# Optimization experiments

Hardware: AMD Instinct MI355X
Metric: run time of the kernel (lower is better)

The kernel has to match this reference:

```python
import jax, jax.numpy as jnp
import numpy as np

NEIGHBORS = 16  # init kwarg 'neighbors'


def _mlp(x, params):
    # SetTransform with reduction='none': pointwise MLP, ReLU between layers, linear output
    for W, b in params[:-1]:
        x = jax.nn.relu(x @ W + b)
    W, b = params[-1]
    return x @ W + b


def setup_inputs() -> dict:
    key = jax.random.key(0)
    B, K, P, DIM, C_IN = 4, 2048, 4096, 3, 64
    C_MID, C_OUT = 32, 128
    WH = 32          # weight_hidden sizes
    FH = 256         # final_hidden size
    FIN = C_IN * C_MID  # 2048, final_conv input

    ks = jax.random.split(key, 16)

    def lin(k, fan_in, fan_out):
        k1, k2 = jax.random.split(k)
        s = 1.0 / np.sqrt(fan_in)
        W = jax.random.uniform(k1, (fan_in, fan_out), minval=-s, maxval=s, dtype=jnp.float32)
        b = jax.random.uniform(k2, (fan_out,), minval=-s, maxval=s, dtype=jnp.float32)
        return W, b

    wc0_W, wc0_b = lin(ks[0], DIM, WH)
    wc1_W, wc1_b = lin(ks[1], WH, WH)
    wc2_W, wc2_b = lin(ks[2], WH, C_MID)
    fc0_W, fc0_b = lin(ks[3], FIN, FH)
    fc1_W, fc1_b = lin(ks[4], FH, C_OUT)

    return {
        "keys": jax.random.normal(ks[5], (B, K, DIM), dtype=jnp.float32),
        "points": jax.random.normal(ks[6], (B, P, DIM), dtype=jnp.float32),
        "feats": jax.random.normal(ks[7], (B, P, C_IN), dtype=jnp.float32),
        "wc0_W": wc0_W, "wc0_b": wc0_b,
        "wc1_W": wc1_W, "wc1_b": wc1_b,
        "wc2_W": wc2_W, "wc2_b": wc2_b,
        "fc0_W": fc0_W, "fc0_b": fc0_b,
        "fc1_W": fc1_W, "fc1_b": fc1_b,
    }


def reference(keys, points, feats,
              wc0_W, wc0_b, wc1_W, wc1_b, wc2_W, wc2_b,
              fc0_W, fc0_b, fc1_W, fc1_b):
    B, K, _ = keys.shape
    # Euclidean dist_fn: rel_pos [B,K,P,dim], squared dist [B,K,P]; all points valid
    dist_vec = points[:, None, :, :] - keys[:, :, None, :]
    dist = jnp.sum(dist_vec * dist_vec, axis=-1)
    # k smallest distances -> neighbor indices [B,K,N]
    _, idxs = jax.lax.top_k(-dist, NEIGHBORS)
    # gather relative positions [B,K,N,dim] and neighbor features [B,K,N,c_in]
    neighbor_rel = jnp.take_along_axis(dist_vec, idxs[..., None], axis=2)
    b_idx = jnp.arange(B)[:, None, None]
    neighbor_feats = feats[b_idx, idxs]
    # per-edge weight MLP: [B,K,N,dim] -> [B,K,N,c_mid]
    m = _mlp(neighbor_rel, [(wc0_W, wc0_b), (wc1_W, wc1_b), (wc2_W, wc2_b)])
    # masked matmul aggregation (all neighbors valid under euclidean dist_fn):
    # m^T @ neighbor_feats -> [B,K,c_mid,c_in], flattened to [B,K,c_mid*c_in]
    e = jnp.einsum('bknm,bknc->bkmc', m, neighbor_feats).reshape(B, K, -1)
    # final pointwise MLP -> [B,K,c_out]
    return _mlp(e, [(fc0_W, fc0_b), (fc1_W, fc1_b)])
```

## Files before the change

### kernel.cpp

```cpp
#include <hip/hip_runtime.h>
#include <cfloat>
#include <climits>

#define BATCH 4
#define KQ    2048
#define NP    4096
#define CIN   64
#define CMID  32
#define NB    16
#define NBINS 4096
#define CANDCAP 256
#define QPB   4

typedef short   bf16x8  __attribute__((ext_vector_type(8)));
typedef float   floatx4 __attribute__((ext_vector_type(4)));

__device__ __forceinline__ unsigned short f2bf(float f) {
  unsigned u = __float_as_uint(f);
  u = (u + 0x7fffu + ((u >> 16) & 1u)) >> 16;
  return (unsigned short)u;
}
__device__ __forceinline__ float bf2f(unsigned short u) {
  return __uint_as_float((unsigned)u << 16);
}

__device__ __forceinline__ void load_lds16(const void* g, void* l) {
  __builtin_amdgcn_global_load_lds(
      (const __attribute__((address_space(1))) unsigned int*)g,
      (__attribute__((address_space(3))) unsigned int*)l, 16, 0, 0);
}

__global__ __launch_bounds__(256, 8) void select_topk(
    const float* __restrict__ keys, const float* __restrict__ points,
    int* __restrict__ nidx_g) {
  __shared__ __align__(16) int hist[NBINS];
  __shared__ int   psum[256];
  __shared__ float cand_d[CANDCAP];
  __shared__ int   cand_i[CANDCAP];
  __shared__ int   nidx[NB];
  __shared__ int   sel_cnt, cand_cnt, sBin, sCbelow;

  const int tid = threadIdx.x;
  const int b   = blockIdx.x >> 11;

#pragma unroll
  for (int t = 0; t < 4; ++t)
    *reinterpret_cast<int4*>(&hist[(tid + t * 256) * 4]) = int4{0, 0, 0, 0};
  if (tid == 0) { sel_cnt = 0; cand_cnt = 0; }

  const float kx = keys[blockIdx.x * 3 + 0];
  const float ky = keys[blockIdx.x * 3 + 1];
  const float kz = keys[blockIdx.x * 3 + 2];
  __syncthreads();

  const float4* pv =
      reinterpret_cast<const float4*>(points + (size_t)b * NP * 3) + (size_t)tid * 12;
  float dreg[16];
#pragma unroll
  for (int g = 0; g < 4; ++g) {
    const float4 v0 = pv[g * 3 + 0];
    const float4 v1 = pv[g * 3 + 1];
    const float4 v2 = pv[g * 3 + 2];
    const float px[4] = {v0.x, v0.w, v1.z, v2.y};
    const float py[4] = {v0.y, v1.x, v1.w, v2.z};
    const float pz[4] = {v0.z, v1.y, v2.x, v2.w};
#pragma unroll
    for (int j = 0; j < 4; ++j) {
      const float dx = px[j] - kx, dy = py[j] - ky, dz = pz[j] - kz;
      const float d  = dx * dx + dy * dy + dz * dz;
      dreg[g * 4 + j] = d;
      atomicAdd(&hist[__float_as_uint(d) >> 19], 1);
    }
  }
  __syncthreads();

  {
    const int base = tid * 16;
    int s = 0;
#pragma unroll
    for (int t = 0; t < 4; ++t) {
      const int4 hv = *reinterpret_cast<const int4*>(&hist[base + t * 4]);
      s += hv.x + hv.y + hv.z + hv.w;
    }
    psum[tid] = s;
  }
  __syncthreads();

  if (tid < 64) {
    const int q = psum[tid * 4] + psum[tid * 4 + 1] + psum[tid * 4 + 2] + psum[tid * 4 + 3];
    int incl = q;
#pragma unroll
    for (int off = 1; off < 64; off <<= 1) {
      int u = __shfl_up(incl, off);
      if (tid >= off) incl += u;
    }
    unsigned long long bal = __ballot(incl >= NB);
    int firstlane = __ffsll((long long)bal) - 1;
    if (tid == firstlane) {
      int cum = incl - q;
      int bin = -1;
      for (int t = 0; t < 4 && bin < 0; ++t) {
        const int ps = psum[tid * 4 + t];
        if (cum + ps >= NB) {
          const int b0 = (tid * 4 + t) * 16;
          for (int j = 0; j < 16; ++j) {
            const int h = hist[b0 + j];
            if (cum + h >= NB) { bin = b0 + j; break; }
            cum += h;
          }
        } else cum += ps;
      }
      sBin = bin; sCbelow = cum;
    }
  }
  __syncthreads();

  const unsigned B = (unsigned)sBin;
#pragma unroll
  for (int j = 0; j < 16; ++j) {
    const int i = tid * 16 + j;
    const unsigned bk = __float_as_uint(dreg[j]) >> 19;
    if (bk < B) {
      int pos = atomicAdd(&sel_cnt, 1);
      nidx[pos] = i;
    } else if (bk == B) {
      int pos = atomicAdd(&cand_cnt, 1);
      if (pos < CANDCAP) { cand_d[pos] = dreg[j]; cand_i[pos] = i; }
    }
  }
  __syncthreads();

  {
    const int rem = NB - sCbelow;
    const int cc  = min(cand_cnt, CANDCAP);
    for (int j = tid; j < cc; j += 256) {
      const float dj = cand_d[j]; const int ij = cand_i[j];
      int rank = 0;
      for (int k = 0; k < cc; ++k) {
        const float dk = cand_d[k]; const int ik = cand_i[k];
        rank += (dk < dj || (dk == dj && ik < ij)) ? 1 : 0;
      }
      if (rank < rem) nidx[sCbelow + rank] = ij;
    }
  }
  __syncthreads();

  if (tid < NB) nidx_g[blockIdx.x * NB + tid] = nidx[tid];
}

__global__ __launch_bounds__(256) void edge_prep(
    const float* __restrict__ keys, const float* __restrict__ points,
    const float* __restrict__ feats, const int* __restrict__ nidx_g,
    const float* __restrict__ wc0_W, const float* __restrict__ wc0_b,
    const float* __restrict__ wc1_W, const float* __restrict__ wc1_b,
    const float* __restrict__ wc2_W, const float* __restrict__ wc2_b,
    const float* __restrict__ fc0_W, const float* __restrict__ fc1_W,
    unsigned short* __restrict__ W0T, unsigned short* __restrict__ W1T,
    unsigned short* __restrict__ E) {
  __shared__ __align__(16) float w0[96], b0v[32], w1[1024], b1v[32], w2[1024], b2v[32];
  __shared__ int   idx_s[QPB * NB];
  __shared__ __align__(16) unsigned short m_bf[QPB * NB][40];
  __shared__ __align__(16) char u_mem[64 * 144];
  float (*h2_all)[36]        = reinterpret_cast<float(*)[36]>(u_mem);
  unsigned short (*f_bf)[72] = reinterpret_cast<unsigned short(*)[72]>(u_mem);
  float (*tt)[33]            = reinterpret_cast<float(*)[33]>(u_mem);

  const int tid = threadIdx.x;
  const int bid = blockIdx.x;
  const int q0  = bid * QPB;
  const int b   = q0 >> 11;

  if (bid < 544) {
    const float* W; unsigned short* WT; int K, N, k0, n0;
    if (bid < 512) { W = fc0_W; WT = W0T; K = 2048; N = 256;
                     k0 = (bid >> 3) * 32; n0 = (bid & 7) * 32; }
    else           { W = fc1_W; WT = W1T; K = 256;  N = 128;
                     k0 = ((bid - 512) >> 2) * 32; n0 = ((bid - 512) & 3) * 32; }
    const int tx = tid & 31, ty = tid >> 5;
#pragma unroll
    for (int p = 0; p < 4; ++p)
      tt[ty + p * 8][tx] = W[(size_t)(k0 + ty + p * 8) * N + n0 + tx];
    __syncthreads();
#pragma unroll
    for (int p = 0; p < 4; ++p)
      WT[(size_t)(n0 + ty + p * 8) * K + k0 + tx] = f2bf(tt[tx][ty + p * 8]);
    __syncthreads();
  }

  if (tid < 96) w0[tid] = wc0_W[tid];
  for (int i = tid; i < 1024; i += 256) { w1[i] = wc1_W[i]; w2[i] = wc2_W[i]; }
  if (tid < 32) { b0v[tid] = wc0_b[tid]; b1v[tid] = wc1_b[tid]; b2v[tid] = wc2_b[tid]; }
  if (tid < QPB * NB) idx_s[tid] = nidx_g[q0 * NB + tid];
  __syncthreads();

  const int edge = tid & 63;
  const int qt   = tid >> 6;
  const int ob   = qt * 8;
  const int qe   = edge >> 4;
  const int idx  = idx_s[edge];
  {
    const float* p  = points + ((size_t)b * NP + idx) * 3;
    const float* kq = keys + (size_t)(q0 + qe) * 3;
    const float rx = p[0] - kq[0], ry = p[1] - kq[1], rz = p[2] - kq[2];

    float h1[32];
#pragma unroll
    for (int o4 = 0; o4 < 8; ++o4) {
      const float4 a = *reinterpret_cast<const float4*>(&w0[o4 * 4]);
      const float4 c = *reinterpret_cast<const float4*>(&w0[32 + o4 * 4]);
      const float4 d = *reinterpret_cast<const float4*>(&w0[64 + o4 * 4]);
      const float4 e = *reinterpret_cast<const float4*>(&b0v[o4 * 4]);
      h1[o4 * 4 + 0] = fmaxf(0.f, rx * a.x + ry * c.x + rz * d.x + e.x);
      h1[o4 * 4 + 1] = fmaxf(0.f, rx * a.y + ry * c.y + rz * d.y + e.y);
      h1[o4 * 4 + 2] = fmaxf(0.f, rx * a.z + ry * c.z + rz * d.z + e.z);
      h1[o4 * 4 + 3] = fmaxf(0.f, rx * a.w + ry * c.w + rz * d.w + e.w);
    }

    float acc2[8];
#pragma unroll
    for (int j = 0; j < 8; ++j) acc2[j] = b1v[ob + j];
#pragma unroll
    for (int i = 0; i < 32; ++i) {
      const float hv = h1[i];
#pragma unroll
      for (int j4 = 0; j4 < 2; ++j4) {
        const float4 w = *reinterpret_cast<const float4*>(&w1[i * 32 + ob + j4 * 4]);
        acc2[j4 * 4 + 0] += hv * w.x;
        acc2[j4 * 4 + 1] += hv * w.y;
        acc2[j4 * 4 + 2] += hv * w.z;
        acc2[j4 * 4 + 3] += hv * w.w;
      }
    }
#pragma unroll
    for (int j4 = 0; j4 < 2; ++j4) {
      float4 o4v;
      o4v.x = fmaxf(acc2[j4 * 4 + 0], 0.f);
      o4v.y = fmaxf(acc2[j4 * 4 + 1], 0.f);
      o4v.z = fmaxf(acc2[j4 * 4 + 2], 0.f);
      o4v.w = fmaxf(acc2[j4 * 4 + 3], 0.f);
      *reinterpret_cast<float4*>(&h2_all[edge][ob + j4 * 4]) = o4v;
    }
  }
  __syncthreads();

  float mo[8];
#pragma unroll
  for (int j = 0; j < 8; ++j) mo[j] = b2v[ob + j];
#pragma unroll
  for (int i = 0; i < 32; ++i) {
    const float hv = h2_all[edge][i];
#pragma unroll
    for (int j4 = 0; j4 < 2; ++j4) {
      const float4 w = *reinterpret_cast<const float4*>(&w2[i * 32 + ob + j4 * 4]);
      mo[j4 * 4 + 0] += hv * w.x;
      mo[j4 * 4 + 1] += hv * w.y;
      mo[j4 * 4 + 2] += hv * w.z;
      mo[j4 * 4 + 3] += hv * w.w;
    }
  }
#pragma unroll
  for (int j = 0; j < 4; ++j) {
    const unsigned lo = f2bf(mo[2 * j]), hi = f2bf(mo[2 * j + 1]);
    *reinterpret_cast<unsigned*>(&m_bf[edge][ob + 2 * j]) = lo | (hi << 16);
  }
  __syncthreads();

#pragma unroll
  for (int t = 0; t < 4; ++t) {
    const int task = tid + t * 256;
    const int row = task >> 4, ch = task & 15;
    const float4 v = *reinterpret_cast<const float4*>(
        feats + ((size_t)b * NP + idx_s[row]) * CIN + ch * 4);
    ushort4 o4;
    o4.x = f2bf(v.x); o4.y = f2bf(v.y); o4.z = f2bf(v.z); o4.w = f2bf(v.w);
    *reinterpret_cast<ushort4*>(&f_bf[row][ch * 4]) = o4;
  }
  __syncthreads();

  const int wv = tid >> 6, lane = tid & 63;
  const int co = lane & 7, mg = lane >> 3;
  {
    const int q = wv;
    float acc[4][8] = {};
#pragma unroll
    for (int n = 0; n < 16; ++n) {
      const int row = q * 16 + n;
      const ushort4 m4 = *reinterpret_cast<const ushort4*>(&m_bf[row][mg * 4]);
      const float mv[4] = {bf2f(m4.x), bf2f(m4.y), bf2f(m4.z), bf2f(m4.w)};
      const uint4 fv = *reinterpret_cast<const uint4*>(&f_bf[row][co * 8]);
      float fc[8];
      fc[0] = __uint_as_float(fv.x << 16); fc[1] = __uint_as_float(fv.x & 0xffff0000u);
      fc[2] = __uint_as_float(fv.y << 16); fc[3] = __uint_as_float(fv.y & 0xffff0000u);
      fc[4] = __uint_as_float(fv.z << 16); fc[5] = __uint_as_float(fv.z & 0xffff0000u);
      fc[6] = __uint_as_float(fv.w << 16); fc[7] = __uint_as_float(fv.w & 0xffff0000u);
#pragma unroll
      for (int i = 0; i < 4; ++i)
#pragma unroll
        for (int j = 0; j < 8; ++j) acc[i][j] += mv[i] * fc[j];
    }
    unsigned short* Eq = E + (size_t)(q0 + q) * 2048;
#pragma unroll
    for (int i = 0; i < 4; ++i) {
      const int mid = mg * 4 + i;
      uint4 o;
      o.x = (unsigned)f2bf(acc[i][0]) | ((unsigned)f2bf(acc[i][1]) << 16);
      o.y = (unsigned)f2bf(acc[i][2]) | ((unsigned)f2bf(acc[i][3]) << 16);
      o.z = (unsigned)f2bf(acc[i][4]) | ((unsigned)f2bf(acc[i][5]) << 16);
      o.w = (unsigned)f2bf(acc[i][6]) | ((unsigned)f2bf(acc[i][7]) << 16);
      *reinterpret_cast<uint4*>(&Eq[mid * 64 + co * 8]) = o;
    }
  }
}

template <int KDIM, bool RELU, bool OUTBF16, bool SWIZZLE>
__global__ __launch_bounds__(256) void gemm_mfma(
    const unsigned short* __restrict__ A,
    const unsigned short* __restrict__ Bt,
    const float* __restrict__ bias,
    void* __restrict__ Cout, int ldc) {
  __shared__ __align__(16) unsigned short Al[2][64 * 128];
  __shared__ __align__(16) unsigned short Bl[2][64 * 128];
  const int tid  = threadIdx.x;
  int m0, n0;
  if (SWIZZLE) {
    const int L    = blockIdx.x;
    const int slot = L >> 3;
    m0 = ((L & 7) * 16 + (slot >> 2)) * 64;
    n0 = (slot & 3) * 64;
  } else {
    m0 = blockIdx.x * 64;
    n0 = blockIdx.y * 64;
  }
  const int wv   = tid >> 6, lane = tid & 63;
  const int quad = lane >> 4, s = lane & 15;
  const int moff = (wv & 1) * 32, noff = (wv >> 1) * 32;
  const int lr   = lane >> 4, lc = lane & 15;

  floatx4 acc[2][2] = {{{0.f,0.f,0.f,0.f},{0.f,0.f,0.f,0.f}},
                       {{0.f,0.f,0.f,0.f},{0.f,0.f,0.f,0.f}}};

  auto stage = [&](int buf, int k0) {
#pragma unroll
    for (int t = 0; t < 4; ++t) {
      const int R0 = wv * 16 + t * 4;
      const int r  = R0 + lr;
      const int gc = lc ^ (r & 7);
      load_lds16(A  + (size_t)(m0 + r) * KDIM + k0 + gc * 8, &Al[buf][R0 * 128]);
      load_lds16(Bt + (size_t)(n0 + r) * KDIM + k0 + gc * 8, &Bl[buf][R0 * 128]);
    }
  };

  auto compute = [&](int buf) {
#pragma unroll
    for (int h = 0; h < 4; ++h) {
      bf16x8 af[2], bfr[2];
#pragma unroll
      for (int i = 0; i < 2; ++i) {
        const int r = moff + i * 16 + s;
        af[i] = *reinterpret_cast<const bf16x8*>(
            &Al[buf][(size_t)r * 128 + ((((h << 2) | quad) ^ (r & 7)) << 3)]);
      }
#pragma unroll
      for (int j = 0; j < 2; ++j) {
        const int r = noff + j * 16 + s;
        bfr[j] = *reinterpret_cast<const bf16x8*>(
            &Bl[buf][(size_t)r * 128 + ((((h << 2) | quad) ^ (r & 7)) << 3)]);
      }
#pragma unroll
      for (int i = 0; i < 2; ++i)
#pragma unroll
        for (int j = 0; j < 2; ++j)
          acc[i][j] = __builtin_amdgcn_mfma_f32_16x16x32_bf16(af[i], bfr[j], acc[i][j], 0, 0, 0);
    }
  };

  constexpr int NT = KDIM / 128;

  stage(0, 0);
  __syncthreads();
  int cur = 0;
#pragma unroll 1
  for (int it = 0; it < NT - 1; ++it) {
    stage(cur ^ 1, (it + 1) * 128);
    compute(cur);
    __syncthreads();
    cur ^= 1;
  }
  compute(cur);

#pragma unroll
  for (int i = 0; i < 2; ++i)
#pragma unroll
    for (int j = 0; j < 2; ++j) {
      const int col = n0 + noff + j * 16 + s;
      const float bv = bias[col];
#pragma unroll
      for (int r = 0; r < 4; ++r) {
        const int row = m0 + moff + i * 16 + quad * 4 + r;
        float v = acc[i][j][r] + bv;
        if (RELU) v = fmaxf(v, 0.f);
        if (OUTBF16)
          ((unsigned short*)Cout)[(size_t)row * ldc + col] = f2bf(v);
        else
          ((float*)Cout)[(size_t)row * ldc + col] = v;
      }
    }
}

extern "C" void kernel_launch(void* const* d_in, const int* in_sizes, int n_in,
                              void* d_out, int out_size, void* d_ws, size_t ws_size,
                              hipStream_t stream) {
  const float* keys   = (const float*)d_in[0];
  const float* points = (const float*)d_in[1];
  const float* feats  = (const float*)d_in[2];
  const float* wc0_W  = (const float*)d_in[3];
  const float* wc0_b  = (const float*)d_in[4];
  const float* wc1_W  = (const float*)d_in[5];
  const float* wc1_b  = (const float*)d_in[6];
  const float* wc2_W  = (const float*)d_in[7];
  const float* wc2_b  = (const float*)d_in[8];
  const float* fc0_W  = (const float*)d_in[9];
  const float* fc0_b  = (const float*)d_in[10];
  const float* fc1_W  = (const float*)d_in[11];
  const float* fc1_b  = (const float*)d_in[12];
  float* out = (float*)d_out;

  const int M = BATCH * KQ;
  char* ws = (char*)d_ws;
  unsigned short* E    = (unsigned short*)(ws);
  unsigned short* H16  = (unsigned short*)(ws + (size_t)33554432);
  unsigned short* W0T  = (unsigned short*)(ws + (size_t)37748736);
  unsigned short* W1T  = (unsigned short*)(ws + (size_t)38797312);
  int*            nidx = (int*)(ws + (size_t)38862848);

  select_topk<<<M, 256, 0, stream>>>(keys, points, nidx);
  edge_prep<<<M / QPB, 256, 0, stream>>>(keys, points, feats, nidx,
                                         wc0_W, wc0_b, wc1_W, wc1_b, wc2_W, wc2_b,
                                         fc0_W, fc1_W, W0T, W1T, E);
  gemm_mfma<2048, true,  true,  true ><<<512, 256, 0, stream>>>(E, W0T, fc0_b, H16, 256);
  gemm_mfma<256,  false, false, false><<<dim3(M / 64, 2), 256, 0, stream>>>(H16, W1T, fc1_b, out, 128);
}
```

Baseline: 170.7 us.

## Rewrite edge MLP and aggregation in edge_prep with per-wave bf16 MFMA

```diff
diff --git a/kernel.cpp b/kernel.cpp
--- a/kernel.cpp
+++ b/kernel.cpp
@@ -157,18 +157,12 @@
     const float* __restrict__ fc0_W, const float* __restrict__ fc1_W,
     unsigned short* __restrict__ W0T, unsigned short* __restrict__ W1T,
     unsigned short* __restrict__ E) {
-  __shared__ __align__(16) float w0[96], b0v[32], w1[1024], b1v[32], w2[1024], b2v[32];
-  __shared__ int   idx_s[QPB * NB];
-  __shared__ __align__(16) unsigned short m_bf[QPB * NB][40];
-  __shared__ __align__(16) char u_mem[64 * 144];
-  float (*h2_all)[36]        = reinterpret_cast<float(*)[36]>(u_mem);
-  unsigned short (*f_bf)[72] = reinterpret_cast<unsigned short(*)[72]>(u_mem);
-  float (*tt)[33]            = reinterpret_cast<float(*)[33]>(u_mem);
+  __shared__ __align__(16) char smem[4 * 5888];
+  float (*tt)[33] = reinterpret_cast<float(*)[33]>(smem);
 
   const int tid = threadIdx.x;
   const int bid = blockIdx.x;
   const int q0  = bid * QPB;
-  const int b   = q0 >> 11;
 
   if (bid < 544) {
     const float* W; unsigned short* WT; int K, N, k0, n0;
@@ -187,127 +181,99 @@
     __syncthreads();
   }
 
-  if (tid < 96) w0[tid] = wc0_W[tid];
-  for (int i = tid; i < 1024; i += 256) { w1[i] = wc1_W[i]; w2[i] = wc2_W[i]; }
-  if (tid < 32) { b0v[tid] = wc0_b[tid]; b1v[tid] = wc1_b[tid]; b2v[tid] = wc2_b[tid]; }
-  if (tid < QPB * NB) idx_s[tid] = nidx_g[q0 * NB + tid];
-  __syncthreads();
-
-  const int edge = tid & 63;
-  const int qt   = tid >> 6;
-  const int ob   = qt * 8;
-  const int qe   = edge >> 4;
-  const int idx  = idx_s[edge];
-  {
-    const float* p  = points + ((size_t)b * NP + idx) * 3;
-    const float* kq = keys + (size_t)(q0 + qe) * 3;
-    const float rx = p[0] - kq[0], ry = p[1] - kq[1], rz = p[2] - kq[2];
-
-    float h1[32];
-#pragma unroll
-    for (int o4 = 0; o4 < 8; ++o4) {
-      const float4 a = *reinterpret_cast<const float4*>(&w0[o4 * 4]);
-      const float4 c = *reinterpret_cast<const float4*>(&w0[32 + o4 * 4]);
-      const float4 d = *reinterpret_cast<const float4*>(&w0[64 + o4 * 4]);
-      const float4 e = *reinterpret_cast<const float4*>(&b0v[o4 * 4]);
-      h1[o4 * 4 + 0] = fmaxf(0.f, rx * a.x + ry * c.x + rz * d.x + e.x);
-      h1[o4 * 4 + 1] = fmaxf(0.f, rx * a.y + ry * c.y + rz * d.y + e.y);
-      h1[o4 * 4 + 2] = fmaxf(0.f, rx * a.z + ry * c.z + rz * d.z + e.z);
-      h1[o4 * 4 + 3] = fmaxf(0.f, rx * a.w + ry * c.w + rz * d.w + e.w);
-    }
-
-    float acc2[8];
-#pragma unroll
-    for (int j = 0; j < 8; ++j) acc2[j] = b1v[ob + j];
-#pragma unroll
-    for (int i = 0; i < 32; ++i) {
-      const float hv = h1[i];
-#pragma unroll
-      for (int j4 = 0; j4 < 2; ++j4) {
-        const float4 w = *reinterpret_cast<const float4*>(&w1[i * 32 + ob + j4 * 4]);
-        acc2[j4 * 4 + 0] += hv * w.x;
-        acc2[j4 * 4 + 1] += hv * w.y;
-        acc2[j4 * 4 + 2] += hv * w.z;
-        acc2[j4 * 4 + 3] += hv * w.w;
-      }
-    }
-#pragma unroll
-    for (int j4 = 0; j4 < 2; ++j4) {
-      float4 o4v;
-      o4v.x = fmaxf(acc2[j4 * 4 + 0], 0.f);
-      o4v.y = fmaxf(acc2[j4 * 4 + 1], 0.f);
-      o4v.z = fmaxf(acc2[j4 * 4 + 2], 0.f);
-      o4v.w = fmaxf(acc2[j4 * 4 + 3], 0.f);
-      *reinterpret_cast<float4*>(&h2_all[edge][ob + j4 * 4]) = o4v;
-    }
-  }
-  __syncthreads();
-
-  float mo[8];
-#pragma unroll
-  for (int j = 0; j < 8; ++j) mo[j] = b2v[ob + j];
-#pragma unroll
-  for (int i = 0; i < 32; ++i) {
-    const float hv = h2_all[edge][i];
-#pragma unroll
-    for (int j4 = 0; j4 < 2; ++j4) {
-      const float4 w = *reinterpret_cast<const float4*>(&w2[i * 32 + ob + j4 * 4]);
-      mo[j4 * 4 + 0] += hv * w.x;
-      mo[j4 * 4 + 1] += hv * w.y;
-      mo[j4 * 4 + 2] += hv * w.z;
-      mo[j4 * 4 + 3] += hv * w.w;
-    }
-  }
-#pragma unroll
-  for (int j = 0; j < 4; ++j) {
-    const unsigned lo = f2bf(mo[2 * j]), hi = f2bf(mo[2 * j + 1]);
-    *reinterpret_cast<unsigned*>(&m_bf[edge][ob + 2 * j]) = lo | (hi << 16);
-  }
-  __syncthreads();
+  const int wv   = tid >> 6, lane = tid & 63;
+  const int s    = lane & 15, g = lane >> 4;
+  const int q    = q0 + wv;
+  const int b    = q >> 11;
+
+  unsigned short* h2s = reinterpret_cast<unsigned short*>(smem + wv * 5888);
+  unsigned short* ms  = reinterpret_cast<unsigned short*>(smem + wv * 5888 + 1280);
+  unsigned short* fsT = reinterpret_cast<unsigned short*>(smem + wv * 5888 + 2816);
+
+  bf16x8 B1[2], B2[2];
+#pragma unroll
+  for (int t = 0; t < 2; ++t) {
+#pragma unroll
+    for (int e = 0; e < 8; ++e) {
+      const int k = 8 * g + e, c = s + 16 * t;
+      B1[t][e] = (short)f2bf(wc1_W[k * 32 + c]);
+      B2[t][e] = (short)f2bf(wc2_W[k * 32 + c]);
+    }
+  }
+
+  const int idx = nidx_g[q * NB + s];
+  const float* p = points + ((size_t)b * NP + idx) * 3;
+  const float kx = keys[q * 3], ky = keys[q * 3 + 1], kz = keys[q * 3 + 2];
+  const float rx = p[0] - kx, ry = p[1] - ky, rz = p[2] - kz;
+  bf16x8 A1;
+#pragma unroll
+  for (int e = 0; e < 8; ++e) {
+    const int j = 8 * g + e;
+    float h = rx * wc0_W[j] + ry * wc0_W[32 + j] + rz * wc0_W[64 + j] + wc0_b[j];
+    A1[e] = (short)f2bf(fmaxf(h, 0.f));
+  }
+
+  const floatx4 zc = {0.f, 0.f, 0.f, 0.f};
+
+#pragma unroll
+  for (int t = 0; t < 2; ++t) {
+    floatx4 d = __builtin_amdgcn_mfma_f32_16x16x32_bf16(A1, B1[t], zc, 0, 0, 0);
+    const float bv = wc1_b[s + 16 * t];
+#pragma unroll
+    for (int r = 0; r < 4; ++r)
+      h2s[(g * 4 + r) * 40 + 16 * t + s] = f2bf(fmaxf(d[r] + bv, 0.f));
+  }
+
+  const bf16x8 A2 = *reinterpret_cast<const bf16x8*>(&h2s[s * 40 + g * 8]);
+
+#pragma unroll
+  for (int t = 0; t < 2; ++t) {
+    floatx4 d = __builtin_amdgcn_mfma_f32_16x16x32_bf16(A2, B2[t], zc, 0, 0, 0);
+    const float bv = wc2_b[s + 16 * t];
+    ushort4 o;
+    o.x = f2bf(d[0] + bv); o.y = f2bf(d[1] + bv);
+    o.z = f2bf(d[2] + bv); o.w = f2bf(d[3] + bv);
+    *reinterpret_cast<ushort4*>(&ms[(16 * t + s) * 24 + g * 4]) = o;
+  }
 
 #pragma unroll
   for (int t = 0; t < 4; ++t) {
-    const int task = tid + t * 256;
-    const int row = task >> 4, ch = task & 15;
+    const int chunk = g + 4 * t;
+    const int n = s;
+    const int idx_n = nidx_g[q * NB + n];
     const float4 v = *reinterpret_cast<const float4*>(
-        feats + ((size_t)b * NP + idx_s[row]) * CIN + ch * 4);
-    ushort4 o4;
-    o4.x = f2bf(v.x); o4.y = f2bf(v.y); o4.z = f2bf(v.z); o4.w = f2bf(v.w);
-    *reinterpret_cast<ushort4*>(&f_bf[row][ch * 4]) = o4;
-  }
-  __syncthreads();
-
-  const int wv = tid >> 6, lane = tid & 63;
-  const int co = lane & 7, mg = lane >> 3;
-  {
-    const int q = wv;
-    float acc[4][8] = {};
-#pragma unroll
-    for (int n = 0; n < 16; ++n) {
-      const int row = q * 16 + n;
-      const ushort4 m4 = *reinterpret_cast<const ushort4*>(&m_bf[row][mg * 4]);
-      const float mv[4] = {bf2f(m4.x), bf2f(m4.y), bf2f(m4.z), bf2f(m4.w)};
-      const uint4 fv = *reinterpret_cast<const uint4*>(&f_bf[row][co * 8]);
-      float fc[8];
-      fc[0] = __uint_as_float(fv.x << 16); fc[1] = __uint_as_float(fv.x & 0xffff0000u);
-      fc[2] = __uint_as_float(fv.y << 16); fc[3] = __uint_as_float(fv.y & 0xffff0000u);
-      fc[4] = __uint_as_float(fv.z << 16); fc[5] = __uint_as_float(fv.z & 0xffff0000u);
-      fc[6] = __uint_as_float(fv.w << 16); fc[7] = __uint_as_float(fv.w & 0xffff0000u);
-#pragma unroll
-      for (int i = 0; i < 4; ++i)
-#pragma unroll
-        for (int j = 0; j < 8; ++j) acc[i][j] += mv[i] * fc[j];
-    }
-    unsigned short* Eq = E + (size_t)(q0 + q) * 2048;
-#pragma unroll
-    for (int i = 0; i < 4; ++i) {
-      const int mid = mg * 4 + i;
-      uint4 o;
-      o.x = (unsigned)f2bf(acc[i][0]) | ((unsigned)f2bf(acc[i][1]) << 16);
-      o.y = (unsigned)f2bf(acc[i][2]) | ((unsigned)f2bf(acc[i][3]) << 16);
-      o.z = (unsigned)f2bf(acc[i][4]) | ((unsigned)f2bf(acc[i][5]) << 16);
-      o.w = (unsigned)f2bf(acc[i][6]) | ((unsigned)f2bf(acc[i][7]) << 16);
-      *reinterpret_cast<uint4*>(&Eq[mid * 64 + co * 8]) = o;
+        feats + ((size_t)b * NP + idx_n) * CIN + chunk * 4);
+    fsT[(chunk * 4 + 0) * 24 + n] = f2bf(v.x);
+    fsT[(chunk * 4 + 1) * 24 + n] = f2bf(v.y);
+    fsT[(chunk * 4 + 2) * 24 + n] = f2bf(v.z);
+    fsT[(chunk * 4 + 3) * 24 + n] = f2bf(v.w);
+  }
+
+  bf16x8 fA[4], mB[2];
+  const bf16x8 zf = {};
+  if (lane < 32) {
+#pragma unroll
+    for (int ct = 0; ct < 4; ++ct)
+      fA[ct] = *reinterpret_cast<const bf16x8*>(&fsT[(ct * 16 + s) * 24 + g * 8]);
+#pragma unroll
+    for (int mt = 0; mt < 2; ++mt)
+      mB[mt] = *reinterpret_cast<const bf16x8*>(&ms[(mt * 16 + s) * 24 + g * 8]);
+  } else {
+#pragma unroll
+    for (int ct = 0; ct < 4; ++ct) fA[ct] = zf;
+#pragma unroll
+    for (int mt = 0; mt < 2; ++mt) mB[mt] = zf;
+  }
+
+  unsigned short* Eq = E + (size_t)q * 2048;
+#pragma unroll
+  for (int mt = 0; mt < 2; ++mt) {
+#pragma unroll
+    for (int ct = 0; ct < 4; ++ct) {
+      floatx4 d = __builtin_amdgcn_mfma_f32_16x16x32_bf16(fA[ct], mB[mt], zc, 0, 0, 0);
+      ushort4 o;
+      o.x = f2bf(d[0]); o.y = f2bf(d[1]); o.z = f2bf(d[2]); o.w = f2bf(d[3]);
+      *reinterpret_cast<ushort4*>(&Eq[(16 * mt + s) * 64 + ct * 16 + g * 4]) = o;
     }
   }
 }
```

Result: faster. 160.6 us (-5.9%).
